# Performance work log

Hardware: AMD Instinct MI355X
Metric: run time of the kernel (lower is better)

## Reference

```python
import jax, jax.numpy as jnp
import numpy as np

B, T_OUT, L, D, H = 1, 8, 512, 512, 8  # batch, frames, tokens/frame, d_model, heads


def setup_inputs() -> dict:
    key = jax.random.key(0)
    ks = jax.random.split(key, 7)
    return {
        "hidden_states": jax.random.normal(ks[0], (B * T_OUT, L, D), jnp.float32),
        "p_out": jax.random.normal(ks[1], (B, T_OUT, 4, 4), jnp.float32),
        "p_out_inv": jax.random.normal(ks[2], (B, T_OUT, 4, 4), jnp.float32),
        "Wq": jax.random.normal(ks[3], (D, D), jnp.float32) * 0.02,
        "Wk": jax.random.normal(ks[4], (D, D), jnp.float32) * 0.02,
        "Wv": jax.random.normal(ks[5], (D, D), jnp.float32) * 0.02,
        "Wo": jax.random.normal(ks[6], (D, D), jnp.float32) * 0.02,
        "bo": jnp.zeros((D,), jnp.float32),
        "num_heads": H,
    }


def cape_embed(f, P):
    # f: (b, S, d), P: (b, S, 4, 4); rearrange '(d k)'->'d k' with k=4, matmul by P, flatten back
    b, S, d = f.shape
    f4 = f.reshape(b, S, d // 4, 4)
    return jnp.einsum('bsdk,bskg->bsdg', f4, P).reshape(b, S, d)


def reference(hidden_states, p_out, p_out_inv, Wq, Wk, Wv, Wo, bo, num_heads):
    b, t_out = p_out.shape[0], p_out.shape[1]
    bt, l, d = hidden_states.shape
    S = t_out * l
    residual = hidden_states

    # '(b t_out) l d -> b (t_out l) d'
    x = hidden_states.reshape(b, S, d)

    q = x @ Wq
    k = x @ Wk
    v = x @ Wv

    # repeat per-frame CAPE matrices over tokens within each frame; self-attn so p_in = p_out
    Pq = jnp.repeat(p_out_inv, l, axis=1)  # (b, S, 4, 4)
    Pk = jnp.repeat(p_out, l, axis=1)      # (b, S, 4, 4)
    q = cape_embed(q, Pq)
    k = cape_embed(k, Pk)

    hd = d // num_heads
    scale = hd ** -0.5
    qh = q.reshape(b, S, num_heads, hd).transpose(0, 2, 1, 3)  # (b, h, S, hd)
    kh = k.reshape(b, S, num_heads, hd).transpose(0, 2, 1, 3)
    vh = v.reshape(b, S, num_heads, hd).transpose(0, 2, 1, 3)

    scores = jnp.einsum('bhqd,bhkd->bhqk', qh, kh) * scale  # full (b,h,S,S) matrix
    probs = jax.nn.softmax(scores, axis=-1)
    o = jnp.einsum('bhqk,bhkd->bhqd', probs, vh)

    o = o.transpose(0, 2, 1, 3).reshape(b, S, d)
    o = o @ Wo + bo  # to_out[0]; to_out[1] dropout is identity in eval

    # 'b (t_out l) d -> (b t_out) l d'
    o = o.reshape(bt, l, d)
    return o + residual  # residual_connection; rescale_output_factor = 1.0
```

## Files before the change

kernel.cpp:

```cpp
#include <hip/hip_runtime.h>
#include <hip/hip_bf16.h>
#include <stdint.h>

typedef __bf16 bf16_t;
typedef __bf16 bf16x2 __attribute__((ext_vector_type(2)));
typedef __bf16 bf16x4 __attribute__((ext_vector_type(4)));
typedef __bf16 bf16x8 __attribute__((ext_vector_type(8)));
typedef float f32x4 __attribute__((ext_vector_type(4)));

#define MFMA(a, b, c) __builtin_amdgcn_mfma_f32_16x16x32_bf16(a, b, c, 0, 0, 0)

#if __has_builtin(__builtin_amdgcn_exp2f)
#define FEXP2 __builtin_amdgcn_exp2f
#else
#define FEXP2 exp2f
#endif

__device__ __forceinline__ void g2lds16(const void* g, void* l) {
  __builtin_amdgcn_global_load_lds(
      reinterpret_cast<const __attribute__((address_space(1))) unsigned int*>(
          reinterpret_cast<uintptr_t>(g)),
      reinterpret_cast<__attribute__((address_space(3))) unsigned int*>(
          reinterpret_cast<uintptr_t>(l)),
      16, 0, 0);
}

__device__ __forceinline__ unsigned cvtpk(float lo, float hi) {
  unsigned r;
  asm("v_cvt_pk_bf16_f32 %0, %1, %2" : "=v"(r) : "v"(lo), "v"(hi));
  return r;
}

__device__ __forceinline__ void lane_swap32(unsigned& a, unsigned& b) {
#if __has_builtin(__builtin_amdgcn_permlane32_swap)
  typedef int i32x2 __attribute__((ext_vector_type(2)));
  i32x2 r = __builtin_amdgcn_permlane32_swap((int)a, (int)b, false, false);
  a = (unsigned)r[0];
  b = (unsigned)r[1];
#else
  asm("v_permlane32_swap_b32 %0, %1" : "+v"(a), "+v"(b));
#endif
}

__device__ __forceinline__ void lane_swap16(unsigned& a, unsigned& b) {
#if __has_builtin(__builtin_amdgcn_permlane16_swap)
  typedef int i32x2 __attribute__((ext_vector_type(2)));
  i32x2 r = __builtin_amdgcn_permlane16_swap((int)a, (int)b, false, false);
  a = (unsigned)r[0];
  b = (unsigned)r[1];
#else
  asm("v_permlane16_swap_b32 %0, %1" : "+v"(a), "+v"(b));
#endif
}

__global__ __launch_bounds__(256) void k_prep(const float* __restrict__ x,
                                              const float* __restrict__ Wq,
                                              const float* __restrict__ Wk,
                                              const float* __restrict__ Wv,
                                              const float* __restrict__ Wo,
                                              const float* __restrict__ Pout,
                                              const float* __restrict__ Pinv,
                                              bf16_t* __restrict__ Xbf,
                                              bf16_t* __restrict__ WqT,
                                              bf16_t* __restrict__ WkT,
                                              bf16_t* __restrict__ WvT,
                                              bf16_t* __restrict__ WoT) {
  const int bid = blockIdx.x;
  if (bid < 2048) {
    int i = (bid * 256 + threadIdx.x) * 4;
    float4 v = *reinterpret_cast<const float4*>(x + i);
    bf16x4 o;
    o[0] = (bf16_t)v.x; o[1] = (bf16_t)v.y; o[2] = (bf16_t)v.z; o[3] = (bf16_t)v.w;
    *reinterpret_cast<bf16x4*>(Xbf + i) = o;
  } else if (bid < 3072) {
    int idx = (bid - 2048) * 256 + threadIdx.x;
    int t = idx >> 15;
    int n = (idx >> 6) & 511;
    int k0 = (idx & 63) << 3;
    int dq4 = (n >> 2) << 2;
    int g = n & 3;
    float pq[4], pk[4];
#pragma unroll
    for (int h = 0; h < 4; ++h) {
      pq[h] = Pinv[t * 16 + h * 4 + g];
      pk[h] = Pout[t * 16 + h * 4 + g];
    }
    bf16x8 oq, ok;
#pragma unroll
    for (int j = 0; j < 8; ++j) {
      const float4 wq = *reinterpret_cast<const float4*>(Wq + (size_t)(k0 + j) * 512 + dq4);
      const float4 wk = *reinterpret_cast<const float4*>(Wk + (size_t)(k0 + j) * 512 + dq4);
      oq[j] = (bf16_t)((wq.x * pq[0] + wq.y * pq[1] + wq.z * pq[2] + wq.w * pq[3]) * 0.1803368801f);
      ok[j] = (bf16_t)(wk.x * pk[0] + wk.y * pk[1] + wk.z * pk[2] + wk.w * pk[3]);
    }
    size_t o = ((size_t)t * 512 + n) * 512 + k0;
    *reinterpret_cast<bf16x8*>(WqT + o) = oq;
    *reinterpret_cast<bf16x8*>(WkT + o) = ok;
  } else {
    int idx = (bid - 3072) * 256 + threadIdx.x;
    int mat = idx >> 15;
    int n = (idx >> 6) & 511;
    int k0 = (idx & 63) << 3;
    const float* W = mat ? Wo : Wv;
    bf16_t* T = mat ? WoT : WvT;
    bf16x8 o;
#pragma unroll
    for (int j = 0; j < 8; ++j) o[j] = (bf16_t)W[(size_t)(k0 + j) * 512 + n];
    *reinterpret_cast<bf16x8*>(T + (size_t)n * 512 + k0) = o;
  }
}

__global__ __launch_bounds__(256) void k_gemm_qkv(const bf16_t* __restrict__ Xbf,
                                                  const bf16_t* __restrict__ WqT,
                                                  const bf16_t* __restrict__ WkT,
                                                  const bf16_t* __restrict__ WvT,
                                                  bf16_t* __restrict__ Qh,
                                                  bf16_t* __restrict__ Kh,
                                                  bf16_t* __restrict__ Vt) {
  __shared__ bf16_t lA[128 * 64];
  __shared__ bf16_t lB[64 * 64];
  const int m0 = blockIdx.x * 128, n0 = blockIdx.y * 64;
  const int mat = blockIdx.z;
  const int frame = m0 >> 9;
  const bf16_t* WT = (mat == 0) ? (WqT + (size_t)frame * 512 * 512)
                   : (mat == 1) ? (WkT + (size_t)frame * 512 * 512)
                                : WvT;
  const int tid = threadIdx.x, lane = tid & 63, wid = tid >> 6;
  const int wr = wid >> 1, wc = wid & 1;
  const int l15 = lane & 15, lg = lane >> 4;
  const int srow = lane >> 3;
  const int scol = ((lane & 7) ^ (lane >> 3)) << 3;

  f32x4 acc[4][2] = {};

  for (int kt = 0; kt < 512; kt += 64) {
#pragma unroll
    for (int i = 0; i < 4; ++i) {
      int chunk = wid * 4 + i;
      int row = chunk * 8 + srow;
      g2lds16(Xbf + (size_t)(m0 + row) * 512 + kt + scol, lA + chunk * 512);
    }
#pragma unroll
    for (int i = 0; i < 2; ++i) {
      int chunk = wid * 2 + i;
      int row = chunk * 8 + srow;
      g2lds16(WT + (size_t)(n0 + row) * 512 + kt + scol, lB + chunk * 512);
    }
    __syncthreads();
#pragma unroll
    for (int kk = 0; kk < 2; ++kk) {
      bf16x8 af[4], bw[2];
      int c16 = ((4 * kk + lg) ^ (l15 & 7)) << 3;
#pragma unroll
      for (int i = 0; i < 4; ++i)
        af[i] = *reinterpret_cast<const bf16x8*>(lA + (wr * 64 + i * 16 + l15) * 64 + c16);
#pragma unroll
      for (int j = 0; j < 2; ++j)
        bw[j] = *reinterpret_cast<const bf16x8*>(lB + (wc * 32 + j * 16 + l15) * 64 + c16);
#pragma unroll
      for (int i = 0; i < 4; ++i)
#pragma unroll
        for (int j = 0; j < 2; ++j)
          acc[i][j] = MFMA(af[i], bw[j], acc[i][j]);
    }
    __syncthreads();
  }

#pragma unroll
  for (int i = 0; i < 4; ++i)
#pragma unroll
    for (int j = 0; j < 2; ++j)
#pragma unroll
      for (int r = 0; r < 4; ++r) {
        int s = m0 + wr * 64 + i * 16 + lg * 4 + r;
        int n = n0 + wc * 32 + j * 16 + l15;
        bf16_t v = (bf16_t)acc[i][j][r];
        if (mat == 2) {
          Vt[(size_t)n * 4096 + s] = v;
        } else if (mat == 0) {
          Qh[((size_t)(n >> 6) * 4096 + s) * 64 + (n & 63)] = v;
        } else {
          Kh[((size_t)(n >> 6) * 4096 + s) * 64 + (n & 63)] = v;
        }
      }
}

__global__ __launch_bounds__(256, 4) void k_attn(const bf16_t* __restrict__ Qh,
                                                 const bf16_t* __restrict__ Kh,
                                                 const bf16_t* __restrict__ Vt,
                                                 char* __restrict__ wsb,
                                                 float* __restrict__ Mp,
                                                 float* __restrict__ Lp) {
  __shared__ bf16_t lK[2][64 * 64];
  __shared__ bf16_t lV[2][64 * 64];
  const int h = blockIdx.y;
  const int ks = blockIdx.z;
  const int q0 = blockIdx.x * 128;
  const int tid = threadIdx.x, lane = tid & 63, wid = tid >> 6;
  const int l15 = lane & 15, lg = lane >> 4;
  const int srow = lane >> 3;
  const int scol = ((lane & 7) ^ (lane >> 3)) << 3;

  bf16_t* Op = (bf16_t*)(ks < 3 ? wsb + ((size_t)ks << 22) : wsb + (29u << 20));

  bf16x8 qf[2][2];
#pragma unroll
  for (int g = 0; g < 2; ++g) {
    const bf16_t* Qp = Qh + ((size_t)h * 4096 + q0 + wid * 32 + g * 16 + l15) * 64;
#pragma unroll
    for (int kk = 0; kk < 2; ++kk)
      qf[g][kk] = *reinterpret_cast<const bf16x8*>(Qp + kk * 32 + lg * 8);
  }

  bf16x8 onesf;
#pragma unroll
  for (int j = 0; j < 8; ++j) onesf[j] = (bf16_t)1.0f;

  const bf16_t* Kb = Kh + ((size_t)h * 4096 + ks * 1024) * 64;
  const bf16_t* Vb = Vt + (size_t)h * 64 * 4096 + ks * 1024;

  f32x4 oT[2][4] = {};
  f32x4 lac[2] = {};
  float m[2] = {-3e38f, -3e38f};

  auto stage = [&](int buf, int kt) {
#pragma unroll
    for (int i = 0; i < 2; ++i) {
      int chunk = wid * 2 + i;
      int row = chunk * 8 + srow;
      g2lds16(Kb + (size_t)(kt + row) * 64 + scol, &lK[buf][chunk * 512]);
      g2lds16(Vb + (size_t)row * 4096 + kt + scol, &lV[buf][chunk * 512]);
    }
  };

  stage(0, 0);
  __syncthreads();

  for (int t = 0; t < 16; ++t) {
    const int cur = t & 1;
    if (t < 15) stage(cur ^ 1, (t + 1) * 64);

    f32x4 st[2][4] = {};
    __builtin_amdgcn_s_setprio(1);
#pragma unroll
    for (int kk = 0; kk < 2; ++kk)
#pragma unroll
      for (int mb = 0; mb < 4; ++mb) {
        bf16x8 kf = *reinterpret_cast<const bf16x8*>(
            &lK[cur][(mb * 16 + l15) * 64 + (((kk * 4 + lg) ^ (l15 & 7)) << 3)]);
        st[0][mb] = MFMA(kf, qf[0][kk], st[0][mb]);
        st[1][mb] = MFMA(kf, qf[1][kk], st[1][mb]);
      }
    __builtin_amdgcn_s_setprio(0);

#pragma unroll
    for (int g = 0; g < 2; ++g) {
      float t0 = fmaxf(fmaxf(st[g][0][0], st[g][0][1]), fmaxf(st[g][0][2], st[g][0][3]));
      float t1 = fmaxf(fmaxf(st[g][1][0], st[g][1][1]), fmaxf(st[g][1][2], st[g][1][3]));
      float t2 = fmaxf(fmaxf(st[g][2][0], st[g][2][1]), fmaxf(st[g][2][2], st[g][2][3]));
      float t3 = fmaxf(fmaxf(st[g][3][0], st[g][3][1]), fmaxf(st[g][3][2], st[g][3][3]));
      float tmax = fmaxf(fmaxf(t0, t1), fmaxf(t2, t3));
      tmax = fmaxf(tmax, __shfl_xor(tmax, 16, 64));
      tmax = fmaxf(tmax, __shfl_xor(tmax, 32, 64));
      if (!__all(tmax <= m[g] + 8.f)) {
        float mnew = fmaxf(m[g], tmax);
        float corr = FEXP2(m[g] - mnew);
        m[g] = mnew;
        lac[g] *= corr;
#pragma unroll
        for (int hb = 0; hb < 4; ++hb) oT[g][hb] *= corr;
      }
#pragma unroll
      for (int mb = 0; mb < 4; ++mb)
#pragma unroll
        for (int r = 0; r < 4; ++r)
          st[g][mb][r] = FEXP2(st[g][mb][r] - m[g]);
    }

    bf16x8 pb[2][2];
#pragma unroll
    for (int g = 0; g < 2; ++g)
#pragma unroll
      for (int kk = 0; kk < 2; ++kk) {
        unsigned A  = cvtpk(st[g][2 * kk][0],     st[g][2 * kk][1]);
        unsigned Ap = cvtpk(st[g][2 * kk][2],     st[g][2 * kk][3]);
        unsigned B  = cvtpk(st[g][2 * kk + 1][0], st[g][2 * kk + 1][1]);
        unsigned Bp = cvtpk(st[g][2 * kk + 1][2], st[g][2 * kk + 1][3]);
        lane_swap32(A, B);
        lane_swap16(A, B);
        lane_swap32(Ap, Bp);
        lane_swap16(Ap, Bp);
        union { unsigned u[4]; bf16x8 v; } pu;
        pu.u[0] = A; pu.u[1] = Ap; pu.u[2] = B; pu.u[3] = Bp;
        pb[g][kk] = pu.v;
      }

    __builtin_amdgcn_s_setprio(1);
#pragma unroll
    for (int kk = 0; kk < 2; ++kk) {
      lac[0] = MFMA(onesf, pb[0][kk], lac[0]);
      lac[1] = MFMA(onesf, pb[1][kk], lac[1]);
#pragma unroll
      for (int hb = 0; hb < 4; ++hb) {
        bf16x8 vf = *reinterpret_cast<const bf16x8*>(
            &lV[cur][(hb * 16 + l15) * 64 + (((kk * 4 + lg) ^ (l15 & 7)) << 3)]);
        oT[0][hb] = MFMA(vf, pb[0][kk], oT[0][hb]);
        oT[1][hb] = MFMA(vf, pb[1][kk], oT[1][hb]);
      }
    }
    __builtin_amdgcn_s_setprio(0);
    __syncthreads();
  }

#pragma unroll
  for (int g = 0; g < 2; ++g) {
    int q = q0 + wid * 32 + g * 16 + l15;
    size_t rbase = ((size_t)ks * 8 + h) * 4096 + q;
    size_t obase = ((size_t)h * 4096 + q) * 64;
    if (lg == 0) { Mp[rbase] = m[g]; Lp[rbase] = lac[g][0]; }
#pragma unroll
    for (int hb = 0; hb < 4; ++hb) {
      bf16x4 ov;
#pragma unroll
      for (int r = 0; r < 4; ++r) ov[r] = (bf16_t)oT[g][hb][r];
      *reinterpret_cast<bf16x4*>(Op + obase + hb * 16 + lg * 4) = ov;
    }
  }
}

__global__ __launch_bounds__(256) void k_merge(char* __restrict__ wsb,
                                               const float* __restrict__ Mp,
                                               const float* __restrict__ Lp,
                                               bf16_t* __restrict__ Obf) {
  int idx = blockIdx.x * 256 + threadIdx.x;
  int d4 = (idx & 15) << 2;
  int row = idx >> 4;
  float ms[4];
  float mstar = -3e38f;
#pragma unroll
  for (int s = 0; s < 4; ++s) {
    ms[s] = Mp[s * 32768 + row];
    mstar = fmaxf(mstar, ms[s]);
  }
  float l = 0.f;
  f32x4 o = {};
#pragma unroll
  for (int s = 0; s < 4; ++s) {
    const bf16_t* Ops = (const bf16_t*)(s < 3 ? wsb + ((size_t)s << 22) : wsb + (29u << 20));
    float w = FEXP2(ms[s] - mstar);
    l += w * Lp[s * 32768 + row];
    bf16x4 v = *reinterpret_cast<const bf16x4*>(Ops + (size_t)row * 64 + d4);
    o[0] += w * (float)v[0]; o[1] += w * (float)v[1];
    o[2] += w * (float)v[2]; o[3] += w * (float)v[3];
  }
  float rinv = 1.f / l;
  int h = row >> 12, q = row & 4095;
  bf16x4 ov;
#pragma unroll
  for (int r = 0; r < 4; ++r) ov[r] = (bf16_t)(o[r] * rinv);
  *reinterpret_cast<bf16x4*>(Obf + (size_t)q * 512 + h * 64 + d4) = ov;
}

__global__ __launch_bounds__(256) void k_gemm_out(const bf16_t* __restrict__ Obf,
                                                  const bf16_t* __restrict__ WoT,
                                                  const float* __restrict__ bo,
                                                  const float* __restrict__ resid,
                                                  float* __restrict__ out) {
  __shared__ bf16_t lA[64 * 64];
  __shared__ bf16_t lB[64 * 64];
  const int m0 = blockIdx.x * 64, n0 = blockIdx.y * 64;
  const int tid = threadIdx.x, lane = tid & 63, wid = tid >> 6;
  const int wr = wid >> 1, wc = wid & 1;
  const int l15 = lane & 15, lg = lane >> 4;
  const int srow = lane >> 3;
  const int scol = ((lane & 7) ^ (lane >> 3)) << 3;

  f32x4 acc[2][2] = {};

  for (int kt = 0; kt < 512; kt += 64) {
#pragma unroll
    for (int i = 0; i < 2; ++i) {
      int chunk = wid * 2 + i;
      int row = chunk * 8 + srow;
      g2lds16(Obf + (size_t)(m0 + row) * 512 + kt + scol, lA + chunk * 512);
      g2lds16(WoT + (size_t)(n0 + row) * 512 + kt + scol, lB + chunk * 512);
    }
    __syncthreads();
#pragma unroll
    for (int kk = 0; kk < 2; ++kk) {
      bf16x8 af[2], bw[2];
      int c16 = ((4 * kk + lg) ^ (l15 & 7)) << 3;
#pragma unroll
      for (int i = 0; i < 2; ++i) {
        af[i] = *reinterpret_cast<const bf16x8*>(lA + (wr * 32 + i * 16 + l15) * 64 + c16);
        bw[i] = *reinterpret_cast<const bf16x8*>(lB + (wc * 32 + i * 16 + l15) * 64 + c16);
      }
#pragma unroll
      for (int i = 0; i < 2; ++i)
#pragma unroll
        for (int j = 0; j < 2; ++j)
          acc[i][j] = MFMA(af[i], bw[j], acc[i][j]);
    }
    __syncthreads();
  }

#pragma unroll
  for (int i = 0; i < 2; ++i)
#pragma unroll
    for (int j = 0; j < 2; ++j)
#pragma unroll
      for (int r = 0; r < 4; ++r) {
        int s = m0 + wr * 32 + i * 16 + lg * 4 + r;
        int n = n0 + wc * 32 + j * 16 + l15;
        size_t o = (size_t)s * 512 + n;
        out[o] = acc[i][j][r] + bo[n] + resid[o];
      }
}

extern "C" void kernel_launch(void* const* d_in, const int* in_sizes, int n_in,
                              void* d_out, int out_size, void* d_ws, size_t ws_size,
                              hipStream_t stream) {
  const float* hs   = (const float*)d_in[0];
  const float* pout = (const float*)d_in[1];
  const float* pinv = (const float*)d_in[2];
  const float* Wq   = (const float*)d_in[3];
  const float* Wk   = (const float*)d_in[4];
  const float* Wv   = (const float*)d_in[5];
  const float* Wo   = (const float*)d_in[6];
  const float* bo   = (const float*)d_in[7];
  float* out = (float*)d_out;

  char* ws = (char*)d_ws;
  bf16_t* Xbf = (bf16_t*)(ws);
  bf16_t* WqT = (bf16_t*)(ws + (4u << 20));
  bf16_t* WkT = (bf16_t*)(ws + (8u << 20));
  bf16_t* WvT = (bf16_t*)(ws + (12u << 20));
  bf16_t* WoT = (bf16_t*)(ws + (12u << 20) + (512u << 10));
  bf16_t* Qh  = (bf16_t*)(ws + (13u << 20));
  bf16_t* Kh  = (bf16_t*)(ws + (17u << 20));
  bf16_t* Vt  = (bf16_t*)(ws + (21u << 20));
  bf16_t* Obf = (bf16_t*)(ws + (25u << 20));
  float*  Mp  = (float*)(ws + (33u << 20));
  float*  Lp  = (float*)(ws + (33u << 20) + (512u << 10));

  hipLaunchKernelGGL(k_prep, dim3(3328), dim3(256), 0, stream,
                     hs, Wq, Wk, Wv, Wo, pout, pinv, Xbf, WqT, WkT, WvT, WoT);
  hipLaunchKernelGGL(k_gemm_qkv, dim3(32, 8, 3), dim3(256), 0, stream,
                     Xbf, WqT, WkT, WvT, Qh, Kh, Vt);
  hipLaunchKernelGGL(k_attn, dim3(32, 8, 4), dim3(256), 0, stream, Qh, Kh, Vt, ws, Mp, Lp);
  hipLaunchKernelGGL(k_merge, dim3(2048), dim3(256), 0, stream, ws, Mp, Lp, Obf);
  hipLaunchKernelGGL(k_gemm_out, dim3(64, 8), dim3(256), 0, stream, Obf, WoT, bo, hs, out);
}
```

Measured before the change: 107.4 us.

## Software-pipeline attention: overlap next QK^T with softmax/PV using 8 waves

The attention kernel now uses 512 threads (8 waves), each owning 16 query rows instead of 32. The loop is software-pipelined so the QK^T MFMAs for tile t+1 are issued before the softmax and PV of tile t, with ping-pong score registers. V gets a triple-buffered LDS ring so the prefetch of tile t+2 does not overwrite V still being read. The aim is to hide exp/softmax latency behind matrix work and raise wave-level parallelism, at the cost of more LDS, more waves per block and higher register pressure under the launch bound.

```diff
diff --git a/kernel.cpp b/kernel.cpp
--- a/kernel.cpp
+++ b/kernel.cpp
@@ -185,14 +185,14 @@
       }
 }
 
-__global__ __launch_bounds__(256, 4) void k_attn(const bf16_t* __restrict__ Qh,
+__global__ __launch_bounds__(512, 4) void k_attn(const bf16_t* __restrict__ Qh,
                                                  const bf16_t* __restrict__ Kh,
                                                  const bf16_t* __restrict__ Vt,
                                                  char* __restrict__ wsb,
                                                  float* __restrict__ Mp,
                                                  float* __restrict__ Lp) {
   __shared__ bf16_t lK[2][64 * 64];
-  __shared__ bf16_t lV[2][64 * 64];
+  __shared__ bf16_t lV[3][64 * 64];
   const int h = blockIdx.y;
   const int ks = blockIdx.z;
   const int q0 = blockIdx.x * 128;
@@ -203,13 +203,12 @@
 
   bf16_t* Op = (bf16_t*)(ks < 3 ? wsb + ((size_t)ks << 22) : wsb + (29u << 20));
 
-  bf16x8 qf[2][2];
-#pragma unroll
-  for (int g = 0; g < 2; ++g) {
-    const bf16_t* Qp = Qh + ((size_t)h * 4096 + q0 + wid * 32 + g * 16 + l15) * 64;
+  bf16x8 qf[2];
+  {
+    const bf16_t* Qp = Qh + ((size_t)h * 4096 + q0 + wid * 16 + l15) * 64;
 #pragma unroll
     for (int kk = 0; kk < 2; ++kk)
-      qf[g][kk] = *reinterpret_cast<const bf16x8*>(Qp + kk * 32 + lg * 8);
+      qf[kk] = *reinterpret_cast<const bf16x8*>(Qp + kk * 32 + lg * 8);
   }
 
   bf16x8 onesf;
@@ -219,110 +218,117 @@
   const bf16_t* Kb = Kh + ((size_t)h * 4096 + ks * 1024) * 64;
   const bf16_t* Vb = Vt + (size_t)h * 64 * 4096 + ks * 1024;
 
-  f32x4 oT[2][4] = {};
-  f32x4 lac[2] = {};
-  float m[2] = {-3e38f, -3e38f};
-
-  auto stage = [&](int buf, int kt) {
-#pragma unroll
-    for (int i = 0; i < 2; ++i) {
-      int chunk = wid * 2 + i;
-      int row = chunk * 8 + srow;
-      g2lds16(Kb + (size_t)(kt + row) * 64 + scol, &lK[buf][chunk * 512]);
-      g2lds16(Vb + (size_t)row * 4096 + kt + scol, &lV[buf][chunk * 512]);
-    }
+  f32x4 oT[4] = {};
+  f32x4 lac = {};
+  float m = -3e38f;
+  f32x4 stA[4], stB[4];
+
+  auto stage = [&](int tt) {
+    int row = wid * 8 + srow;
+    g2lds16(Kb + (size_t)(tt * 64 + row) * 64 + scol, &lK[tt & 1][wid * 512]);
+    g2lds16(Vb + (size_t)row * 4096 + tt * 64 + scol, &lV[tt % 3][wid * 512]);
   };
 
-  stage(0, 0);
-  __syncthreads();
-
-  for (int t = 0; t < 16; ++t) {
-    const int cur = t & 1;
-    if (t < 15) stage(cur ^ 1, (t + 1) * 64);
-
-    f32x4 st[2][4] = {};
+  auto qk = [&](f32x4(&st)[4], int tt) {
+    const bf16_t* base = lK[tt & 1];
     __builtin_amdgcn_s_setprio(1);
+#pragma unroll
+    for (int mb = 0; mb < 4; ++mb) st[mb] = f32x4{};
 #pragma unroll
     for (int kk = 0; kk < 2; ++kk)
 #pragma unroll
       for (int mb = 0; mb < 4; ++mb) {
         bf16x8 kf = *reinterpret_cast<const bf16x8*>(
-            &lK[cur][(mb * 16 + l15) * 64 + (((kk * 4 + lg) ^ (l15 & 7)) << 3)]);
-        st[0][mb] = MFMA(kf, qf[0][kk], st[0][mb]);
-        st[1][mb] = MFMA(kf, qf[1][kk], st[1][mb]);
+            base + (mb * 16 + l15) * 64 + (((kk * 4 + lg) ^ (l15 & 7)) << 3));
+        st[mb] = MFMA(kf, qf[kk], st[mb]);
       }
     __builtin_amdgcn_s_setprio(0);
-
-#pragma unroll
-    for (int g = 0; g < 2; ++g) {
-      float t0 = fmaxf(fmaxf(st[g][0][0], st[g][0][1]), fmaxf(st[g][0][2], st[g][0][3]));
-      float t1 = fmaxf(fmaxf(st[g][1][0], st[g][1][1]), fmaxf(st[g][1][2], st[g][1][3]));
-      float t2 = fmaxf(fmaxf(st[g][2][0], st[g][2][1]), fmaxf(st[g][2][2], st[g][2][3]));
-      float t3 = fmaxf(fmaxf(st[g][3][0], st[g][3][1]), fmaxf(st[g][3][2], st[g][3][3]));
-      float tmax = fmaxf(fmaxf(t0, t1), fmaxf(t2, t3));
-      tmax = fmaxf(tmax, __shfl_xor(tmax, 16, 64));
-      tmax = fmaxf(tmax, __shfl_xor(tmax, 32, 64));
-      if (!__all(tmax <= m[g] + 8.f)) {
-        float mnew = fmaxf(m[g], tmax);
-        float corr = FEXP2(m[g] - mnew);
-        m[g] = mnew;
-        lac[g] *= corr;
-#pragma unroll
-        for (int hb = 0; hb < 4; ++hb) oT[g][hb] *= corr;
-      }
-#pragma unroll
-      for (int mb = 0; mb < 4; ++mb)
-#pragma unroll
-        for (int r = 0; r < 4; ++r)
-          st[g][mb][r] = FEXP2(st[g][mb][r] - m[g]);
-    }
-
-    bf16x8 pb[2][2];
-#pragma unroll
-    for (int g = 0; g < 2; ++g)
-#pragma unroll
-      for (int kk = 0; kk < 2; ++kk) {
-        unsigned A  = cvtpk(st[g][2 * kk][0],     st[g][2 * kk][1]);
-        unsigned Ap = cvtpk(st[g][2 * kk][2],     st[g][2 * kk][3]);
-        unsigned B  = cvtpk(st[g][2 * kk + 1][0], st[g][2 * kk + 1][1]);
-        unsigned Bp = cvtpk(st[g][2 * kk + 1][2], st[g][2 * kk + 1][3]);
-        lane_swap32(A, B);
-        lane_swap16(A, B);
-        lane_swap32(Ap, Bp);
-        lane_swap16(Ap, Bp);
-        union { unsigned u[4]; bf16x8 v; } pu;
-        pu.u[0] = A; pu.u[1] = Ap; pu.u[2] = B; pu.u[3] = Bp;
-        pb[g][kk] = pu.v;
-      }
-
+  };
+
+  auto smppv = [&](f32x4(&st)[4], int tt) {
+    float t0 = fmaxf(fmaxf(st[0][0], st[0][1]), fmaxf(st[0][2], st[0][3]));
+    float t1 = fmaxf(fmaxf(st[1][0], st[1][1]), fmaxf(st[1][2], st[1][3]));
+    float t2 = fmaxf(fmaxf(st[2][0], st[2][1]), fmaxf(st[2][2], st[2][3]));
+    float t3 = fmaxf(fmaxf(st[3][0], st[3][1]), fmaxf(st[3][2], st[3][3]));
+    float tmax = fmaxf(fmaxf(t0, t1), fmaxf(t2, t3));
+    tmax = fmaxf(tmax, __shfl_xor(tmax, 16, 64));
+    tmax = fmaxf(tmax, __shfl_xor(tmax, 32, 64));
+    if (!__all(tmax <= m + 8.f)) {
+      float mnew = fmaxf(m, tmax);
+      float corr = FEXP2(m - mnew);
+      m = mnew;
+      lac *= corr;
+#pragma unroll
+      for (int hb = 0; hb < 4; ++hb) oT[hb] *= corr;
+    }
+#pragma unroll
+    for (int mb = 0; mb < 4; ++mb)
+#pragma unroll
+      for (int r = 0; r < 4; ++r)
+        st[mb][r] = FEXP2(st[mb][r] - m);
+
+    bf16x8 pb[2];
+#pragma unroll
+    for (int kk = 0; kk < 2; ++kk) {
+      unsigned A  = cvtpk(st[2 * kk][0],     st[2 * kk][1]);
+      unsigned Ap = cvtpk(st[2 * kk][2],     st[2 * kk][3]);
+      unsigned B  = cvtpk(st[2 * kk + 1][0], st[2 * kk + 1][1]);
+      unsigned Bp = cvtpk(st[2 * kk + 1][2], st[2 * kk + 1][3]);
+      lane_swap32(A, B);
+      lane_swap16(A, B);
+      lane_swap32(Ap, Bp);
+      lane_swap16(Ap, Bp);
+      union { unsigned u[4]; bf16x8 v; } pu;
+      pu.u[0] = A; pu.u[1] = Ap; pu.u[2] = B; pu.u[3] = Bp;
+      pb[kk] = pu.v;
+    }
+
+    const bf16_t* vbase = lV[tt % 3];
     __builtin_amdgcn_s_setprio(1);
 #pragma unroll
     for (int kk = 0; kk < 2; ++kk) {
-      lac[0] = MFMA(onesf, pb[0][kk], lac[0]);
-      lac[1] = MFMA(onesf, pb[1][kk], lac[1]);
+      lac = MFMA(onesf, pb[kk], lac);
 #pragma unroll
       for (int hb = 0; hb < 4; ++hb) {
         bf16x8 vf = *reinterpret_cast<const bf16x8*>(
-            &lV[cur][(hb * 16 + l15) * 64 + (((kk * 4 + lg) ^ (l15 & 7)) << 3)]);
-        oT[0][hb] = MFMA(vf, pb[0][kk], oT[0][hb]);
-        oT[1][hb] = MFMA(vf, pb[1][kk], oT[1][hb]);
+            vbase + (hb * 16 + l15) * 64 + (((kk * 4 + lg) ^ (l15 & 7)) << 3));
+        oT[hb] = MFMA(vf, pb[kk], oT[hb]);
       }
     }
     __builtin_amdgcn_s_setprio(0);
-    __syncthreads();
-  }
-
-#pragma unroll
-  for (int g = 0; g < 2; ++g) {
-    int q = q0 + wid * 32 + g * 16 + l15;
+  };
+
+  stage(0);
+  __syncthreads();
+  qk(stA, 0);
+  stage(1);
+
+  for (int i = 0; i < 7; ++i) {
+    const int t = 2 * i;
+    __syncthreads();
+    qk(stB, t + 1);
+    stage(t + 2);
+    smppv(stA, t);
+    __syncthreads();
+    qk(stA, t + 2);
+    stage(t + 3);
+    smppv(stB, t + 1);
+  }
+  __syncthreads();
+  qk(stB, 15);
+  smppv(stA, 14);
+  smppv(stB, 15);
+
+  {
+    int q = q0 + wid * 16 + l15;
     size_t rbase = ((size_t)ks * 8 + h) * 4096 + q;
     size_t obase = ((size_t)h * 4096 + q) * 64;
-    if (lg == 0) { Mp[rbase] = m[g]; Lp[rbase] = lac[g][0]; }
+    if (lg == 0) { Mp[rbase] = m; Lp[rbase] = lac[0]; }
 #pragma unroll
     for (int hb = 0; hb < 4; ++hb) {
       bf16x4 ov;
 #pragma unroll
-      for (int r = 0; r < 4; ++r) ov[r] = (bf16_t)oT[g][hb][r];
+      for (int r = 0; r < 4; ++r) ov[r] = (bf16_t)oT[hb][r];
       *reinterpret_cast<bf16x4*>(Op + obase + hb * 16 + lg * 4) = ov;
     }
   }
@@ -447,7 +453,7 @@
                      hs, Wq, Wk, Wv, Wo, pout, pinv, Xbf, WqT, WkT, WvT, WoT);
   hipLaunchKernelGGL(k_gemm_qkv, dim3(32, 8, 3), dim3(256), 0, stream,
                      Xbf, WqT, WkT, WvT, Qh, Kh, Vt);
-  hipLaunchKernelGGL(k_attn, dim3(32, 8, 4), dim3(256), 0, stream, Qh, Kh, Vt, ws, Mp, Lp);
+  hipLaunchKernelGGL(k_attn, dim3(32, 8, 4), dim3(512), 0, stream, Qh, Kh, Vt, ws, Mp, Lp);
   hipLaunchKernelGGL(k_merge, dim3(2048), dim3(256), 0, stream, ws, Mp, Lp, Obf);
   hipLaunchKernelGGL(k_gemm_out, dim3(64, 8), dim3(256), 0, stream, Obf, WoT, bo, hs, out);
 }
```

New measurement: 108.5 us. No clear change (+1.0%).
